# Kernel tuning notes

Hardware: AMD Instinct MI355X
Metric: run time of the kernel (lower is better)

The kernel has to match this reference:

```python
import jax, jax.numpy as jnp
import numpy as np

L = 32      # in_capsules
O = 32      # out_capsules
P = 16      # p_size
PD = 4      # p_dim = sqrt(p_size)
ETA = 1.0


def setup_inputs() -> dict:
    key = jax.random.key(0)
    k1, k2 = jax.random.split(key)
    # [B, H, W, L*16 + L]
    input_tensor = jax.random.normal(k1, (16, 14, 14, L * P + L), dtype=jnp.float32)
    # torch param: [1, K*K*L, O, 4, 4] with kernel_size=1
    weights = jax.random.normal(k2, (1, L, O, PD, PD), dtype=jnp.float32) * 0.25
    activation_bias = jnp.full((O,), 0.1, dtype=jnp.float32)
    return {"input_tensor": input_tensor, "weights": weights,
            "activation_bias": activation_bias}


def reference(input_tensor, weights, activation_bias):
    B = input_tensor.shape[0]
    # split poses / activations along channel dim
    poses_in = input_tensor[..., :-L].reshape(B, -1, PD, PD)   # [B, N, 4, 4], N = H*W*L
    acts_in = input_tensor[..., -L:].reshape(B, -1)            # [B, N]
    N = poses_in.shape[1]

    # share_transform: tile weights over spatial positions (H*W copies of the L blocks)
    w = jnp.tile(weights[0], (N // L, 1, 1, 1))                # [N, O, 4, 4]
    votes = jnp.einsum('bnij,nojk->bnoik', poses_in, w)        # [B, N, O, 4, 4]
    votes = votes.reshape(B, N, O, P)                          # [B, N, O, 16]

    # spectral routing
    votes = acts_in[:, :, None, None] * votes                  # weight by child activations
    votes = jnp.transpose(votes, (0, 2, 1, 3))                 # [B, O, N, 16]

    # top-1 right singular vector via eigendecomposition of the 16x16 gram matrix
    gram = jnp.einsum('bonp,bonq->bopq', votes, votes)         # [B, O, 16, 16]
    _, vecs = jnp.linalg.eigh(gram)                            # ascending eigenvalues
    poses = jax.lax.stop_gradient(vecs[..., -1])               # [B, O, 16] (detached, as in torch)

    yu = jnp.einsum('bonp,bop->bon', votes, poses)             # [B, O, N]
    yu_norm_sq = jnp.sum(yu * yu, axis=-1)                     # [B, O]
    y_fro_sq = jnp.sum(votes * votes, axis=(-1, -2))           # [B, O]
    activations = jax.nn.sigmoid(ETA * (yu_norm_sq / y_fro_sq - activation_bias))
    return activations, poses
```

## Files before the change

kernel.cpp:

```cpp
#include <hip/hip_runtime.h>
#include <hip/hip_bf16.h>


#define NSPAT 196

__device__ __forceinline__ float wsum64(float x) {
  x += __shfl_xor(x, 32);
  x += __shfl_xor(x, 16);
  x += __shfl_xor(x, 8);
  x += __shfl_xor(x, 4);
  x += __shfl_xor(x, 2);
  x += __shfl_xor(x, 1);
  return x;
}

__device__ __forceinline__ float rlanef(float x, int i) {
  return __int_as_float(__builtin_amdgcn_readlane(__float_as_int(x), i));
}

__global__ __launch_bounds__(256) void moments_kernel(const float* __restrict__ in,
                                                      float* __restrict__ Mout) {
  int b = blockIdx.x >> 5;
  int l = blockIdx.x & 31;
  __shared__ float ps[NSPAT][16];
  __shared__ float as2[NSPAT];
  int t = threadIdx.x;
  for (int j = t; j < NSPAT * 16; j += 256) {
    int s = j >> 4, p = j & 15;
    ps[s][p] = in[((size_t)(b * NSPAT + s)) * 544 + l * 16 + p];
  }
  for (int s = t; s < NSPAT; s += 256) {
    float a = in[((size_t)(b * NSPAT + s)) * 544 + 512 + l];
    as2[s] = a * a;
  }
  __syncthreads();
  int p = t >> 4, q = t & 15;
  float acc = 0.f;
  for (int s = 0; s < NSPAT; ++s) {
    acc += as2[s] * (ps[s][p] * ps[s][q]);
  }
  Mout[(size_t)blockIdx.x * 256 + t] = acc;
}

__global__ __launch_bounds__(256) void gram_kernel(const float* __restrict__ Min,
                                                   const float* __restrict__ W,
                                                   float* __restrict__ Gout) {
  int b = blockIdx.x >> 5;
  int o = blockIdx.x & 31;
  int t = threadIdx.x;
  __shared__ float Ms[32][256];
  __shared__ float Ws[32][16];
  for (int l = 0; l < 32; ++l)
    Ms[l][t] = Min[((size_t)(b * 32 + l)) * 256 + t];
  for (int j = t; j < 32 * 16; j += 256)
    Ws[j >> 4][j & 15] = W[((size_t)((j >> 4) * 32 + o)) * 16 + (j & 15)];
  __syncthreads();
  int p = t >> 4, q = t & 15;
  int i1 = p >> 2, k1 = p & 3, i2 = q >> 2, k2 = q & 3;
  float acc = 0.f;
  for (int l = 0; l < 32; ++l) {
    float sub = 0.f;
    for (int j2 = 0; j2 < 4; ++j2) {
      float inner = 0.f;
      for (int j = 0; j < 4; ++j)
        inner += Ws[l][j * 4 + k1] * Ms[l][(i1 * 4 + j) * 16 + (i2 * 4 + j2)];
      sub += Ws[l][j2 * 4 + k2] * inner;
    }
    acc += sub;
  }
  Gout[(size_t)blockIdx.x * 256 + t] = acc;
}

#define EPSF    5.9604645e-08f
#define EPS2F   (EPSF * EPSF)
#define SAFMINF 1.1754944e-38f

__device__ __forceinline__ float ssign(float a, float b) {
  return (b >= 0.f) ? fabsf(a) : -fabsf(a);
}

__device__ __forceinline__ float slapy2(float x, float y) {
  float xa = fabsf(x), ya = fabsf(y);
  float w = fmaxf(xa, ya), z = fminf(xa, ya);
  if (z == 0.f) return w;
  float t = z / w;
  return w * sqrtf(1.f + t * t);
}

__device__ __forceinline__ void slartg(float f, float g, float* c, float* s, float* r) {
  if (g == 0.f) {
    *c = 1.f; *s = 0.f; *r = f;
  } else if (f == 0.f) {
    *c = 0.f; *s = (g >= 0.f) ? 1.f : -1.f; *r = fabsf(g);
  } else {
    float d = sqrtf(f * f + g * g);
    *c = fabsf(f) / d;
    float rr = (f >= 0.f) ? d : -d;
    *s = g / rr;
    *r = rr;
  }
}

__device__ __forceinline__ void slaev2(float a, float b, float c,
                                       float* rt1, float* rt2, float* cs1, float* sn1) {
  float sm = a + c;
  float df = a - c;
  float adf = fabsf(df);
  float tb = b + b;
  float ab = fabsf(tb);
  float acmx, acmn;
  if (fabsf(a) > fabsf(c)) { acmx = a; acmn = c; } else { acmx = c; acmn = a; }
  float rt;
  if (adf > ab)      { float t = ab / adf; rt = adf * sqrtf(1.f + t * t); }
  else if (adf < ab) { float t = adf / ab; rt = ab * sqrtf(1.f + t * t); }
  else               { rt = ab * sqrtf(2.f); }
  int sgn1;
  if (sm < 0.f) {
    *rt1 = 0.5f * (sm - rt); sgn1 = -1;
    *rt2 = (acmx / *rt1) * acmn - (b / *rt1) * b;
  } else if (sm > 0.f) {
    *rt1 = 0.5f * (sm + rt); sgn1 = 1;
    *rt2 = (acmx / *rt1) * acmn - (b / *rt1) * b;
  } else {
    *rt1 = 0.5f * rt; *rt2 = -0.5f * rt; sgn1 = 1;
  }
  float cs; int sgn2;
  if (df >= 0.f) { cs = df + rt; sgn2 = 1; }
  else           { cs = df - rt; sgn2 = -1; }
  float acs = fabsf(cs);
  float c1, s1;
  if (acs > ab) {
    float ct = -tb / cs;
    s1 = 1.f / sqrtf(1.f + ct * ct);
    c1 = ct * s1;
  } else {
    if (ab == 0.f) { c1 = 1.f; s1 = 0.f; }
    else {
      float tn = -cs / tb;
      c1 = 1.f / sqrtf(1.f + tn * tn);
      s1 = tn * c1;
    }
  }
  if (sgn1 == sgn2) { float tn = c1; c1 = -s1; s1 = tn; }
  *cs1 = c1; *sn1 = s1;
}

#define MAXLOG 1024

__global__ __launch_bounds__(64) void eig_kernel(const float* __restrict__ G,
                                                 const float* __restrict__ bias,
                                                 float* __restrict__ out) {
  const int pid = blockIdx.x;
  const int lane = threadIdx.x;
  const int row = lane & 15;
  __shared__ float A[16][17];
  __shared__ float ddl[64][17];
  __shared__ float eel[64][17];
  __shared__ float ttl[64][17];
  __shared__ float2 logcs[MAXLOG];
  __shared__ int    logi[MAXLOG];

  for (int k = 0; k < 4; ++k) {
    int t = lane + 64 * k;
    int r = t >> 4, c = t & 15;
    int rr = r >= c ? r : c;
    int cc = r >= c ? c : r;
    A[r][c] = G[(size_t)pid * 256 + rr * 16 + cc];
  }
  float trc = (lane < 16) ? G[(size_t)pid * 256 + lane * 17] : 0.f;
  float trace = wsum64(trc);
  __syncthreads();

  for (int i = 0; i < 15; ++i) {
    float acol = (lane < 16) ? A[lane][i] : 0.f;
    float alpha = __shfl(acol, i + 1);
    float x = (lane >= i + 2 && lane < 16) ? acol : 0.f;
    float xns = wsum64(x * x);
    if (xns == 0.f) {
      eel[lane][i] = alpha;
      ttl[lane][i] = 0.f;
      continue;
    }
    float beta = (alpha >= 0.f ? -1.f : 1.f) * sqrtf(alpha * alpha + xns);
    float taui = (beta - alpha) / beta;
    float scal = 1.f / (alpha - beta);
    float vreg = 0.f;
    if (lane == i + 1) vreg = 1.f;
    else if (lane >= i + 2 && lane < 16) {
      vreg = acol * scal;
      A[lane][i] = vreg;
    }
    eel[lane][i] = beta;
    ttl[lane][i] = taui;
    float wr = 0.f;
    for (int cI = i + 1; cI < 16; ++cI) {
      float vc = __shfl(vreg, cI);
      if (lane >= i + 1 && lane < 16) wr += A[lane][cI] * vc;
    }
    wr *= taui;
    float dot = wsum64((lane >= i + 1 && lane < 16) ? wr * vreg : 0.f);
    float alpha2 = -0.5f * taui * dot;
    wr += alpha2 * vreg;
    for (int cI = i + 1; cI < 16; ++cI) {
      float wc = __shfl(wr, cI);
      float vc = __shfl(vreg, cI);
      if (lane >= i + 1 && lane < 16) A[lane][cI] -= vreg * wc + wr * vc;
    }
  }

  float di = (lane < 16) ? A[lane][lane] : 0.f;
  for (int j = 0; j < 16; ++j) ddl[lane][j] = __shfl(di, j);

  float* dd = ddl[lane];
  float* ee = eel[lane];
  ee[15] = 0.f;

  int m, l, lsv, lend, lendsv;
  int jtot = 0;
  const int nmaxit = 16 * 30;
  int l1 = 0;
  int nrot = 0;
  float dsn, esn;

outer:
  if (l1 > 15) goto done;
  if (l1 > 0) ee[l1 - 1] = 0.f;
  dsn = dd[row];
  esn = ee[row];
  {
    int mm;
    for (mm = l1; mm < 15; ++mm) {
      float eI = rlanef(esn, mm);
      float tst = fabsf(eI);
      if (tst == 0.f) break;
      if (tst <= (sqrtf(fabsf(rlanef(dsn, mm))) * sqrtf(fabsf(rlanef(dsn, mm + 1)))) * EPSF) {
        ee[mm] = 0.f;
        break;
      }
    }
    m = mm;
  }
  l = l1; lsv = l; lend = m; lendsv = lend;
  l1 = m + 1;
  if (lend == l) goto outer;
  {
    float an = 0.f;
    for (int k2 = l; k2 <= lend; ++k2) an = fmaxf(an, fabsf(rlanef(dsn, k2)));
    for (int k2 = l; k2 < lend; ++k2) an = fmaxf(an, fabsf(rlanef(esn, k2)));
    if (an == 0.f) goto outer;
  }
  if (fabsf(rlanef(dsn, lend)) < fabsf(rlanef(dsn, l))) { lend = lsv; l = lendsv; }

  if (lend > l) {
ql_top:
    dsn = dd[row];
    esn = ee[row];
    {
      int mm;
      for (mm = l; mm < lend; ++mm) {
        float eI = rlanef(esn, mm);
        float tst = eI * eI;
        if (tst <= (EPS2F * fabsf(rlanef(dsn, mm))) * fabsf(rlanef(dsn, mm + 1)) + SAFMINF) break;
      }
      m = mm;
    }
    if (m < lend) ee[m] = 0.f;
    {
      float p = rlanef(dsn, l);
      if (m == l) {
        dd[l] = p;
        l = l + 1;
        if (l <= lend) goto ql_top;
        goto blk_done;
      }
      if (m == l + 1) {
        float rt1, rt2, c2, s2;
        slaev2(rlanef(dsn, l), rlanef(esn, l), rlanef(dsn, l + 1), &rt1, &rt2, &c2, &s2);
        if (lane == 0 && nrot < MAXLOG) { logcs[nrot] = make_float2(c2, -s2); logi[nrot] = l; }
        nrot++;
        dd[l] = rt1; dd[l + 1] = rt2; ee[l] = 0.f;
        l += 2;
        if (l <= lend) goto ql_top;
        goto blk_done;
      }
      if (jtot == nmaxit) goto blk_done;
      jtot++;
      float g = (rlanef(dsn, l + 1) - p) / (2.f * rlanef(esn, l));
      float r = slapy2(g, 1.f);
      g = rlanef(dsn, m) - p + rlanef(esn, l) / (g + ssign(r, g));
      float s = 1.f, c = 1.f;
      p = 0.f;
      for (int i = m - 1; i >= l; --i) {
        float eI = rlanef(esn, i);
        float f = s * eI;
        float bb = c * eI;
        slartg(g, f, &c, &s, &r);
        if (i != m - 1) ee[i + 1] = r;
        g = rlanef(dsn, i + 1) - p;
        r = (rlanef(dsn, i) - g) * s + 2.f * c * bb;
        p = s * r;
        dd[i + 1] = g + p;
        g = c * r - bb;
        if (lane == 0 && nrot < MAXLOG) { logcs[nrot] = make_float2(c, s); logi[nrot] = i; }
        nrot++;
      }
      dd[l] = rlanef(dsn, l) - p;
      ee[l] = g;
    }
    goto ql_top;
  } else {
qr_top:
    dsn = dd[row];
    esn = ee[row];
    {
      int mm;
      for (mm = l; mm > lend; --mm) {
        float eI = rlanef(esn, mm - 1);
        float tst = eI * eI;
        if (tst <= (EPS2F * fabsf(rlanef(dsn, mm))) * fabsf(rlanef(dsn, mm - 1)) + SAFMINF) break;
      }
      m = mm;
    }
    if (m > lend) ee[m - 1] = 0.f;
    {
      float p = rlanef(dsn, l);
      if (m == l) {
        dd[l] = p;
        l = l - 1;
        if (l >= lend) goto qr_top;
        goto blk_done;
      }
      if (m == l - 1) {
        float rt1, rt2, c2, s2;
        slaev2(rlanef(dsn, l - 1), rlanef(esn, l - 1), rlanef(dsn, l), &rt1, &rt2, &c2, &s2);
        if (lane == 0 && nrot < MAXLOG) { logcs[nrot] = make_float2(c2, -s2); logi[nrot] = l - 1; }
        nrot++;
        dd[l - 1] = rt1; dd[l] = rt2; ee[l - 1] = 0.f;
        l -= 2;
        if (l >= lend) goto qr_top;
        goto blk_done;
      }
      if (jtot == nmaxit) goto blk_done;
      jtot++;
      float g = (rlanef(dsn, l - 1) - p) / (2.f * rlanef(esn, l - 1));
      float r = slapy2(g, 1.f);
      g = rlanef(dsn, m) - p + rlanef(esn, l - 1) / (g + ssign(r, g));
      float s = 1.f, c = 1.f;
      p = 0.f;
      for (int i = m; i <= l - 1; ++i) {
        float eI = rlanef(esn, i);
        float f = s * eI;
        float bb = c * eI;
        slartg(g, f, &c, &s, &r);
        if (i != m) ee[i - 1] = r;
        g = rlanef(dsn, i) - p;
        r = (rlanef(dsn, i + 1) - g) * s + 2.f * c * bb;
        p = s * r;
        dd[i] = g + p;
        g = c * r - bb;
        if (lane == 0 && nrot < MAXLOG) { logcs[nrot] = make_float2(c, -s); logi[nrot] = i; }
        nrot++;
      }
      dd[l] = rlanef(dsn, l) - p;
      ee[l - 1] = g;
    }
    goto qr_top;
  }
blk_done:
  goto outer;

done:;
  dsn = dd[row];
  int kmax = 0;
  float dmax = rlanef(dsn, 0);
  for (int j = 1; j < 16; ++j) {
    float dj = rlanef(dsn, j);
    if (dj > dmax) { dmax = dj; kmax = j; }
  }

  float w = (lane == kmax) ? 1.f : 0.f;
  {
    int t = nrot - 1;
    if (t > MAXLOG - 1) t = MAXLOG - 1;
    while (t >= 0) {
      int base = t & ~63;
      float2 cs = logcs[base + lane];
      int ii = logi[base + lane];
      for (int k = t - base; k >= 0; --k) {
        float c = rlanef(cs.x, k);
        float sg = rlanef(cs.y, k);
        int i = __builtin_amdgcn_readlane(ii, k);
        float wup = __shfl_up(w, 1);
        float wdn = __shfl_down(w, 1);
        float nw = w;
        if (lane == i) nw = c * w + sg * wdn;
        else if (lane == i + 1) nw = -sg * wup + c * w;
        w = nw;
      }
      t = base - 1;
    }
  }

  float vreg = (lane < 16) ? w : 0.f;
  for (int i = 14; i >= 0; --i) {
    float taui = ttl[lane][i];
    if (taui == 0.f) continue;
    float contrib;
    if (lane == i + 1) contrib = vreg;
    else if (lane >= i + 2 && lane < 16) contrib = A[lane][i] * vreg;
    else contrib = 0.f;
    float dot = wsum64(contrib);
    float td = taui * dot;
    if (lane == i + 1) vreg -= td;
    else if (lane >= i + 2 && lane < 16) vreg -= td * A[lane][i];
  }

  float act = 1.f / (1.f + expf(-(dmax / trace - bias[pid & 31])));
  if (lane == 0) out[pid] = act;
  if (lane < 16) out[512 + pid * 16 + lane] = vreg;
}

extern "C" void kernel_launch(void* const* d_in, const int* in_sizes, int n_in,
                              void* d_out, int out_size, void* d_ws, size_t ws_size,
                              hipStream_t stream) {
  const float* in   = (const float*)d_in[0];
  const float* W    = (const float*)d_in[1];
  const float* bias = (const float*)d_in[2];
  float* out = (float*)d_out;

  float* Mbuf = (float*)d_ws;
  float* Gbuf = Mbuf + 512 * 256;

  moments_kernel<<<512, 256, 0, stream>>>(in, Mbuf);
  gram_kernel<<<512, 256, 0, stream>>>(Mbuf, W, Gbuf);
  eig_kernel<<<512, 64, 0, stream>>>(Gbuf, bias, out);
}
```

Measured before the change: 257.0 us.

## Fuse gram computation into eigen kernel, computing only lower triangle

Removes the separate gram kernel and computes the 16x16 gram matrix inside the eigen kernel. The kernel loads the per-batch moments and weights into shared memory and evaluates only the 136 lower-triangle entries, mirroring each one into the upper half. This saves a kernel launch and the global round-trip of the gram buffer, and halves the gram arithmetic. In exchange each 64-lane eigen block now loads 32 KB of moments with only 64 threads and needs much more shared memory, which may lower occupancy.

Measured after the change: 267.7 us. 4.2% more time.

```diff
diff --git a/kernel.cpp b/kernel.cpp
--- a/kernel.cpp
+++ b/kernel.cpp
@@ -40,35 +40,6 @@
     acc += as2[s] * (ps[s][p] * ps[s][q]);
   }
   Mout[(size_t)blockIdx.x * 256 + t] = acc;
-}
-
-__global__ __launch_bounds__(256) void gram_kernel(const float* __restrict__ Min,
-                                                   const float* __restrict__ W,
-                                                   float* __restrict__ Gout) {
-  int b = blockIdx.x >> 5;
-  int o = blockIdx.x & 31;
-  int t = threadIdx.x;
-  __shared__ float Ms[32][256];
-  __shared__ float Ws[32][16];
-  for (int l = 0; l < 32; ++l)
-    Ms[l][t] = Min[((size_t)(b * 32 + l)) * 256 + t];
-  for (int j = t; j < 32 * 16; j += 256)
-    Ws[j >> 4][j & 15] = W[((size_t)((j >> 4) * 32 + o)) * 16 + (j & 15)];
-  __syncthreads();
-  int p = t >> 4, q = t & 15;
-  int i1 = p >> 2, k1 = p & 3, i2 = q >> 2, k2 = q & 3;
-  float acc = 0.f;
-  for (int l = 0; l < 32; ++l) {
-    float sub = 0.f;
-    for (int j2 = 0; j2 < 4; ++j2) {
-      float inner = 0.f;
-      for (int j = 0; j < 4; ++j)
-        inner += Ws[l][j * 4 + k1] * Ms[l][(i1 * 4 + j) * 16 + (i2 * 4 + j2)];
-      sub += Ws[l][j2 * 4 + k2] * inner;
-    }
-    acc += sub;
-  }
-  Gout[(size_t)blockIdx.x * 256 + t] = acc;
 }
 
 #define EPSF    5.9604645e-08f
@@ -147,12 +118,17 @@
 
 #define MAXLOG 1024
 
-__global__ __launch_bounds__(64) void eig_kernel(const float* __restrict__ G,
+__global__ __launch_bounds__(64) void eig_kernel(const float* __restrict__ Min,
+                                                 const float* __restrict__ W,
                                                  const float* __restrict__ bias,
                                                  float* __restrict__ out) {
   const int pid = blockIdx.x;
+  const int b = pid >> 5;
+  const int o = pid & 31;
   const int lane = threadIdx.x;
   const int row = lane & 15;
+  __shared__ float Ms[32][256];
+  __shared__ float Ws[32][16];
   __shared__ float A[16][17];
   __shared__ float ddl[64][17];
   __shared__ float eel[64][17];
@@ -160,16 +136,35 @@
   __shared__ float2 logcs[MAXLOG];
   __shared__ int    logi[MAXLOG];
 
-  for (int k = 0; k < 4; ++k) {
-    int t = lane + 64 * k;
-    int r = t >> 4, c = t & 15;
-    int rr = r >= c ? r : c;
-    int cc = r >= c ? c : r;
-    A[r][c] = G[(size_t)pid * 256 + rr * 16 + cc];
-  }
-  float trc = (lane < 16) ? G[(size_t)pid * 256 + lane * 17] : 0.f;
+  for (int j = lane; j < 32 * 256; j += 64)
+    ((float*)Ms)[j] = Min[(size_t)b * 8192 + j];
+  for (int j = lane; j < 32 * 16; j += 64)
+    Ws[j >> 4][j & 15] = W[((size_t)((j >> 4) * 32 + o)) * 16 + (j & 15)];
+  __syncthreads();
+
+  for (int idx = lane; idx < 136; idx += 64) {
+    int r = 0;
+    while ((r + 1) * (r + 2) / 2 <= idx) ++r;
+    int c = idx - r * (r + 1) / 2;
+    int i1 = r >> 2, k1 = r & 3, i2 = c >> 2, k2 = c & 3;
+    float acc = 0.f;
+    for (int l = 0; l < 32; ++l) {
+      float sub = 0.f;
+      for (int j2 = 0; j2 < 4; ++j2) {
+        float inner = 0.f;
+        for (int j = 0; j < 4; ++j)
+          inner += Ws[l][j * 4 + k1] * Ms[l][(i1 * 4 + j) * 16 + (i2 * 4 + j2)];
+        sub += Ws[l][j2 * 4 + k2] * inner;
+      }
+      acc += sub;
+    }
+    A[r][c] = acc;
+    A[c][r] = acc;
+  }
+  __syncthreads();
+
+  float trc = (lane < 16) ? A[lane][lane] : 0.f;
   float trace = wsum64(trc);
-  __syncthreads();
 
   for (int i = 0; i < 15; ++i) {
     float acol = (lane < 16) ? A[lane][i] : 0.f;
@@ -429,9 +424,7 @@
   float* out = (float*)d_out;
 
   float* Mbuf = (float*)d_ws;
-  float* Gbuf = Mbuf + 512 * 256;
 
   moments_kernel<<<512, 256, 0, stream>>>(in, Mbuf);
-  gram_kernel<<<512, 256, 0, stream>>>(Mbuf, W, Gbuf);
-  eig_kernel<<<512, 64, 0, stream>>>(Gbuf, bias, out);
-}
+  eig_kernel<<<512, 64, 0, stream>>>(Mbuf, W, bias, out);
+}
```
